# Performance work log

Hardware: AMD Instinct MI355X
Metric: run time of the kernel (lower is better)

## Reference

```python
import math
import jax, jax.numpy as jnp
import numpy as np
from jax import lax

B, T, D = 2, 2048, 1024
H, W, E = 16, 16, 8
HD = D // H


def setup_inputs() -> dict:
    key = jax.random.key(0)
    ks = jax.random.split(key, 9)
    s = 0.02
    return {
        "x": jax.random.normal(ks[0], (B, T, D), dtype=jnp.float32),
        # CausalConv1d weights: torch Conv1d layout [out_ch, in_ch, kernel]
        "q_w": jax.random.normal(ks[1], (D, D, W), dtype=jnp.float32) * s,
        "q_b": jax.random.normal(ks[2], (D,), dtype=jnp.float32) * s,
        "k_w": jax.random.normal(ks[3], (D, D, W), dtype=jnp.float32) * s,
        "k_b": jax.random.normal(ks[4], (D,), dtype=jnp.float32) * s,
        # Linear weights: torch layout [out, in]
        "v_w": jax.random.normal(ks[5], (D, D), dtype=jnp.float32) * s,
        "v_b": jax.random.normal(ks[6], (D,), dtype=jnp.float32) * s,
        "p_w": jax.random.normal(ks[7], (D, D), dtype=jnp.float32) * s,
        "p_b": jax.random.normal(ks[8], (D,), dtype=jnp.float32) * s,
    }


def _causal_conv(x_t, w, b):
    # x_t: [B, D, T]; left-pad by W-1 so output at t sees inputs <= t
    xp = jnp.pad(x_t, ((0, 0), (0, 0), (W - 1, 0)))
    y = lax.conv_general_dilated(xp, w, window_strides=(1,), padding="VALID",
                                 dimension_numbers=("NCH", "OIH", "NCH"))
    return y + b[None, :, None]


def _split_heads(z):
    # [B, T, D] -> [B, H, T, hd]
    return z.reshape(B, T, H, HD).transpose(0, 2, 1, 3)


def reference(x, q_w, q_b, k_w, k_b, v_w, v_b, p_w, p_b):
    x_t = x.transpose(0, 2, 1)  # [B, D, T]
    q = _split_heads(_causal_conv(x_t, q_w, q_b).transpose(0, 2, 1))
    k = _split_heads(_causal_conv(x_t, k_w, k_b).transpose(0, 2, 1))
    v = _split_heads(jnp.einsum("btd,od->bto", x, v_w) + v_b)
    scale = 1.0 / math.sqrt(HD)

    # ---- local window attention (unfold equivalent) ----
    # zero-pad keys/values W-1 steps to the left along T, gather sliding windows
    k_pad = jnp.pad(k, ((0, 0), (0, 0), (W - 1, 0), (0, 0)))
    v_pad = jnp.pad(v, ((0, 0), (0, 0), (W - 1, 0), (0, 0)))
    widx = jnp.arange(T)[:, None] + jnp.arange(W)[None, :]  # [T, W]
    patches_k = k_pad[:, :, widx]  # [B, H, T, W, hd]
    patches_v = v_pad[:, :, widx]  # [B, H, T, W, hd]
    attn_l = jax.nn.softmax(jnp.einsum("bhtd,bhtwd->bhtw", q, patches_k) * scale, axis=-1)
    out_l = jnp.einsum("bhtw,bhtwd->bhtd", attn_l, patches_v)

    # ---- exponential jumps: roll by 2^e (wrap-around, as in original) ----
    out_e = jnp.zeros_like(out_l)
    for e in range(E):
        shift = 2 ** e
        if shift >= T:
            break
        k_s = jnp.roll(k, -shift, axis=2)
        v_s = jnp.roll(v, -shift, axis=2)
        score = jnp.sum(q * k_s, axis=-1) * scale  # [B, H, T]
        alpha = jax.nn.softmax(score, axis=-1)[..., None]  # softmax over T (faithful)
        out_e = out_e + alpha * v_s

    out = (out_l + out_e).transpose(0, 2, 1, 3).reshape(B, T, D)
    return jnp.einsum("btd,od->bto", out, p_w) + p_b
```

## Files before the change

### kernel.cpp

```cpp
#include <hip/hip_runtime.h>
#include <cstdint>
#include <cstddef>

#define TSEQ 2048
#define DDIM 1024

typedef _Float16 f16;
typedef _Float16 f16x2 __attribute__((ext_vector_type(2)));
typedef _Float16 f16x4 __attribute__((ext_vector_type(4)));
typedef _Float16 f16x8 __attribute__((ext_vector_type(8)));
typedef float f32x4 __attribute__((ext_vector_type(4)));


__device__ __align__(16) static const unsigned char g_zero16[16] = {};

__device__ __forceinline__ void gload_lds16(const void* g, void* l) {
  __builtin_amdgcn_global_load_lds(
      (const __attribute__((address_space(1))) void*)g,
      (__attribute__((address_space(3))) void*)l, 16, 0, 0);
}

__global__ void cvt_all(const float* __restrict__ x, const float* __restrict__ vw,
                        const float* __restrict__ pw,
                        f16* __restrict__ xh, f16* __restrict__ vwh, f16* __restrict__ pwh) {
  int b = blockIdx.x;
  const float* src; f16* dst; int i;
  if (b < 4096)      { src = x;  dst = xh;  i = b * 256 + threadIdx.x; }
  else if (b < 5120) { src = vw; dst = vwh; i = (b - 4096) * 256 + threadIdx.x; }
  else               { src = pw; dst = pwh; i = (b - 5120) * 256 + threadIdx.x; }
  float4 v = ((const float4*)src)[i];
  f16x4 h = { (f16)v.x, (f16)v.y, (f16)v.z, (f16)v.w };
  ((f16x4*)dst)[i] = h;
}

__global__ __launch_bounds__(256) void cvt_w_tr(const float* __restrict__ qw,
                                                const float* __restrict__ kw,
                                                f16* __restrict__ qd, f16* __restrict__ kd) {
  __shared__ f16 tile[16][1032];
  const int o = blockIdx.x;
  const float* src; f16* dst;
  if (o < 1024) { src = qw + (size_t)o * 16384; dst = qd + (size_t)o * 16384; }
  else          { src = kw + (size_t)(o - 1024) * 16384; dst = kd + (size_t)(o - 1024) * 16384; }
  const int tid = threadIdx.x;
  #pragma unroll
  for (int p = 0; p < 16; p++) {
    const int idx = p * 256 + tid;
    const int i = idx >> 2, wq = idx & 3;
    float4 v = *(const float4*)(src + (size_t)i * 16 + wq * 4);
    tile[wq * 4 + 0][i] = (f16)v.x;
    tile[wq * 4 + 1][i] = (f16)v.y;
    tile[wq * 4 + 2][i] = (f16)v.z;
    tile[wq * 4 + 3][i] = (f16)v.w;
  }
  __syncthreads();
  #pragma unroll
  for (int p = 0; p < 8; p++) {
    const int c = p * 256 + tid;
    const int w = c >> 7, i8 = (c & 127) * 8;
    *(f16x8*)(dst + (size_t)w * 1024 + i8) = *(const f16x8*)&tile[w][i8];
  }
}

__global__ __launch_bounds__(512, 1) void gemm_qk8(
    const f16* __restrict__ xh,
    const f16* __restrict__ Bq, const f16* __restrict__ Bk,
    const float* __restrict__ bq, const float* __restrict__ bk,
    f16* __restrict__ oq, f16* __restrict__ ok)
{
  extern __shared__ __align__(16) f16 smem[];
  const int tid = threadIdx.x;
  const int lane = tid & 63;
  const int wid = tid >> 6;
  const int wq = wid >> 1;
  const int wp = wid & 1;

  const int m0 = blockIdx.x * 256;
  const int n0 = blockIdx.y * 64;
  const int bT = m0 & ~(TSEQ - 1);
  const int t0 = m0 & (TSEQ - 1);

  const int srow = lane >> 3;
  const int chunk8 = (((lane & 7) ^ (srow & 7)) << 3);

  f32x4 acc[4][4] = {};

  auto stageA = [&](int kt, int buf) {
    const int kk = kt << 6;
    const int w = kk >> 10;
    const int i0 = kk & (DDIM - 1);
    f16* sb = smem + buf * 24576;
    #pragma unroll
    for (int c = 0; c < 4; c++) {
      const int rr = wid * 32 + c * 8;
      const int srcT = t0 + rr + srow + w - 15;
      const void* g = (srcT >= 0)
          ? (const void*)(xh + (((size_t)(bT + srcT)) << 10) + i0 + chunk8)
          : (const void*)g_zero16;
      gload_lds16(g, (void*)&sb[rr * 64]);
    }
  };
  auto stageB = [&](int kt, int buf) {
    const int kk = kt << 6;
    f16* sb = smem + buf * 24576 + (wid < 4 ? 16384 : 20480);
    const f16* Bsrc = (wid < 4) ? Bq : Bk;
    const int wb = wid & 3;
    #pragma unroll
    for (int c = 0; c < 2; c++) {
      const int rr = wb * 16 + c * 8;
      const void* g = (const void*)(Bsrc + (((size_t)(n0 + rr + srow)) << 14) + kk + chunk8);
      gload_lds16(g, (void*)&sb[rr * 64]);
    }
  };

  stageA(0, 0); stageB(0, 0);
  stageA(1, 1); stageB(1, 1);

  const int NT = 16384 / 64;
  int buf = 0;
  for (int kt = 0; kt < NT; kt++) {
    if (kt < NT - 1) {
      asm volatile("s_waitcnt vmcnt(6)" ::: "memory");
    } else {
      asm volatile("s_waitcnt vmcnt(0)" ::: "memory");
    }
    __builtin_amdgcn_s_barrier();
    __builtin_amdgcn_sched_barrier(0);

    const f16* sb = smem + buf * 24576;
    const f16* bsb = sb + (wp ? 20480 : 16384);
    const int stq = kt + 2;
    const int sbuf = (buf >= 1) ? buf - 1 : 2;

    {
      const int slot = (((lane >> 4)) ^ (lane & 7)) << 3;
      f16x8 af[4], bf[4];
      #pragma unroll
      for (int i = 0; i < 4; i++)
        af[i] = *(const f16x8*)&sb[(wq * 64 + i * 16 + (lane & 15)) * 64 + slot];
      #pragma unroll
      for (int j = 0; j < 4; j++)
        bf[j] = *(const f16x8*)&bsb[(j * 16 + (lane & 15)) * 64 + slot];
      if (stq < NT) stageA(stq, sbuf);
      __builtin_amdgcn_s_barrier();
      asm volatile("s_waitcnt lgkmcnt(0)" ::: "memory");
      __builtin_amdgcn_sched_barrier(0);
      __builtin_amdgcn_s_setprio(1);
      #pragma unroll
      for (int i = 0; i < 4; i++)
        #pragma unroll
        for (int j = 0; j < 4; j++)
          acc[i][j] = __builtin_amdgcn_mfma_f32_16x16x32_f16(af[i], bf[j], acc[i][j], 0, 0, 0);
      __builtin_amdgcn_s_setprio(0);
    }

    {
      const int slot = ((4 + (lane >> 4)) ^ (lane & 7)) << 3;
      f16x8 af[4], bf[4];
      #pragma unroll
      for (int i = 0; i < 4; i++)
        af[i] = *(const f16x8*)&sb[(wq * 64 + i * 16 + (lane & 15)) * 64 + slot];
      #pragma unroll
      for (int j = 0; j < 4; j++)
        bf[j] = *(const f16x8*)&bsb[(j * 16 + (lane & 15)) * 64 + slot];
      if (stq < NT) stageB(stq, sbuf);
      __builtin_amdgcn_s_barrier();
      asm volatile("s_waitcnt lgkmcnt(0)" ::: "memory");
      __builtin_amdgcn_sched_barrier(0);
      __builtin_amdgcn_s_setprio(1);
      #pragma unroll
      for (int i = 0; i < 4; i++)
        #pragma unroll
        for (int j = 0; j < 4; j++)
          acc[i][j] = __builtin_amdgcn_mfma_f32_16x16x32_f16(af[i], bf[j], acc[i][j], 0, 0, 0);
      __builtin_amdgcn_s_setprio(0);
    }

    buf = (buf == 2) ? 0 : buf + 1;
  }

  const int crow = (lane >> 4) << 2;
  const int ccol = lane & 15;
  const int hh = n0 >> 6;
  const float* bias = wp ? bk : bq;
  f16* outp = wp ? ok : oq;
  #pragma unroll
  for (int j = 0; j < 4; j++) {
    const int col = n0 + j * 16 + ccol;
    const float bvl = bias[col];
    const int d = (j << 4) + ccol;
    #pragma unroll
    for (int i = 0; i < 4; i++) {
      #pragma unroll
      for (int r = 0; r < 4; r++) {
        const int row = m0 + wq * 64 + i * 16 + crow + r;
        const int b = row >> 11, t = row & (TSEQ - 1);
        outp[((size_t)(b * 16 + hh) * TSEQ + t) * 64 + d] = (f16)(acc[i][j][r] + bvl);
      }
    }
  }
}

template<int MODE>
__global__ __launch_bounds__(256, 2) void gemm_small(
    const f16* __restrict__ A, const f16* __restrict__ Bw,
    const float* __restrict__ bias, f16* __restrict__ oh, float* __restrict__ ofp)
{
  __shared__ f16 As[128 * 32];
  __shared__ f16 Bs[128 * 32];
  const int tid = threadIdx.x;
  const int lane = tid & 63;
  const int wid = tid >> 6;
  const int m0 = blockIdx.x * 128;
  const int n0 = blockIdx.y * 128;

  const int srow = lane >> 2;
  const int scg = ((lane & 3) ^ ((lane >> 3) & 3)) * 8;
  const int wm = wid & 1;
  const int wn = wid >> 1;

  f32x4 acc[4][4] = {};

  for (int kk = 0; kk < 1024; kk += 32) {
    __syncthreads();
    if (wid < 2) {
      #pragma unroll
      for (int c = 0; c < 4; c++) {
        const int r = wid * 64 + c * 16 + srow;
        const void* g = (const void*)(A + (((size_t)(m0 + r)) << 10) + kk + scg);
        gload_lds16(g, (void*)&As[(wid * 64 + c * 16) * 32]);
      }
    } else {
      #pragma unroll
      for (int c = 0; c < 4; c++) {
        const int r = (wid - 2) * 64 + c * 16 + srow;
        const void* g = (const void*)(Bw + (((size_t)(n0 + r)) << 10) + kk + scg);
        gload_lds16(g, (void*)&Bs[((wid - 2) * 64 + c * 16) * 32]);
      }
    }
    __syncthreads();
    const int koff = ((lane >> 4) ^ ((lane >> 1) & 3)) * 8;
    f16x8 af[4], bf[4];
    #pragma unroll
    for (int i = 0; i < 4; i++) {
      af[i] = *(const f16x8*)&As[(wm * 64 + i * 16 + (lane & 15)) * 32 + koff];
      bf[i] = *(const f16x8*)&Bs[(wn * 64 + i * 16 + (lane & 15)) * 32 + koff];
    }
    #pragma unroll
    for (int i = 0; i < 4; i++)
      #pragma unroll
      for (int j = 0; j < 4; j++)
        acc[i][j] = __builtin_amdgcn_mfma_f32_16x16x32_f16(af[i], bf[j], acc[i][j], 0, 0, 0);
  }

  const int crow = (lane >> 4) * 4;
  const int ccol = lane & 15;
  #pragma unroll
  for (int j = 0; j < 4; j++) {
    const int col = n0 + wn * 64 + j * 16 + ccol;
    const float bvl = bias[col];
    #pragma unroll
    for (int i = 0; i < 4; i++) {
      #pragma unroll
      for (int r = 0; r < 4; r++) {
        const int row = m0 + wm * 64 + i * 16 + crow + r;
        const float val = acc[i][j][r] + bvl;
        if (MODE == 1) {
          ofp[(size_t)row * DDIM + col] = val;
        } else {
          const int b = row >> 11, t = row & (TSEQ - 1);
          const int h = col >> 6, d = col & 63;
          oh[((size_t)(b * 16 + h) * TSEQ + t) * 64 + d] = (f16)val;
        }
      }
    }
  }
}

__global__ __launch_bounds__(256) void score_k(const f16* __restrict__ qh,
                                               const f16* __restrict__ kh,
                                               float* __restrict__ scores) {
  const int bid = blockIdx.x;
  const int bh = bid >> 5, tc = bid & 31;
  const int tid = threadIdx.x;
  const int wave = tid >> 6, lane = tid & 63;
  const int tr = lane >> 3, dc = lane & 7;
  const size_t base = ((size_t)bh) << 17;
  const f16* qb = qh + base;
  const f16* kb = kh + base;

  #pragma unroll
  for (int p = 0; p < 2; p++) {
    const int t = tc * 64 + p * 32 + wave * 8 + tr;
    f16x8 qv = *(const f16x8*)(qb + (size_t)t * 64 + dc * 8);
    const f16x2* qp = (const f16x2*)&qv;
    #pragma unroll
    for (int e = 0; e < 8; e++) {
      const int ts = (t + (1 << e)) & (TSEQ - 1);
      f16x8 kv = *(const f16x8*)(kb + (size_t)ts * 64 + dc * 8);
      const f16x2* kp = (const f16x2*)&kv;
      float s = 0.f;
      #pragma unroll
      for (int j = 0; j < 4; j++) s = __builtin_amdgcn_fdot2(qp[j], kp[j], s, false);
      s += __shfl_xor(s, 1, 64);
      s += __shfl_xor(s, 2, 64);
      s += __shfl_xor(s, 4, 64);
      if (dc == 0) scores[((size_t)(bh * 8 + e) << 11) + t] = s * 0.125f;
    }
  }
}

__global__ void softmax_k(float* __restrict__ scores) {
  __shared__ float red[4];
  int row = blockIdx.x;
  float* p = scores + ((size_t)row << 11);
  int tid = threadIdx.x;
  float v[8];
  float4 a = ((const float4*)p)[tid * 2];
  float4 b = ((const float4*)p)[tid * 2 + 1];
  v[0] = a.x; v[1] = a.y; v[2] = a.z; v[3] = a.w;
  v[4] = b.x; v[5] = b.y; v[6] = b.z; v[7] = b.w;
  float m = v[0];
  #pragma unroll
  for (int j = 1; j < 8; j++) m = fmaxf(m, v[j]);
  for (int o = 32; o > 0; o >>= 1) m = fmaxf(m, __shfl_xor(m, o, 64));
  if ((tid & 63) == 0) red[tid >> 6] = m;
  __syncthreads();
  m = fmaxf(fmaxf(red[0], red[1]), fmaxf(red[2], red[3]));
  __syncthreads();
  float s = 0.f;
  #pragma unroll
  for (int j = 0; j < 8; j++) { v[j] = __expf(v[j] - m); s += v[j]; }
  for (int o = 32; o > 0; o >>= 1) s += __shfl_xor(s, o, 64);
  if ((tid & 63) == 0) red[tid >> 6] = s;
  __syncthreads();
  s = (red[0] + red[1]) + (red[2] + red[3]);
  float inv = 1.0f / s;
  float4 o1 = make_float4(v[0] * inv, v[1] * inv, v[2] * inv, v[3] * inv);
  float4 o2 = make_float4(v[4] * inv, v[5] * inv, v[6] * inv, v[7] * inv);
  ((float4*)p)[tid * 2] = o1;
  ((float4*)p)[tid * 2 + 1] = o2;
}

__global__ __launch_bounds__(256) void attn_out_k(
    const f16* __restrict__ qh, const f16* __restrict__ kh, const f16* __restrict__ vh,
    const float* __restrict__ alpha, f16* __restrict__ outh)
{
  __shared__ f16 qL[64 * 64];
  __shared__ f16 kL[80 * 64];
  __shared__ f16 vL[208 * 64];
  __shared__ float scL[64 * 16];
  __shared__ float aL[8 * 64];
  const int bh = blockIdx.x, tc = blockIdx.y;
  const int t0 = tc * 64;
  const int tid = threadIdx.x;
  const size_t base = ((size_t)bh) << 17;

  for (int idx = tid; idx < 64 * 8; idx += 256) {
    int r = idx >> 3, c = idx & 7, sl = c ^ (r & 7);
    *(uint4*)&qL[r * 64 + sl * 8] = *(const uint4*)(qh + base + (size_t)(t0 + r) * 64 + c * 8);
  }
  for (int idx = tid; idx < 79 * 8; idx += 256) {
    int r = idx >> 3, c = idx & 7, sl = c ^ (r & 7);
    int g = t0 - 15 + r;
    uint4 val = (g < 0) ? make_uint4(0, 0, 0, 0)
                        : *(const uint4*)(kh + base + (size_t)g * 64 + c * 8);
    *(uint4*)&kL[r * 64 + sl * 8] = val;
  }
  for (int idx = tid; idx < 207 * 8; idx += 256) {
    int r = idx >> 3, c = idx & 7, sl = c ^ (r & 7);
    int g = t0 - 15 + r;
    uint4 val;
    if (g < 0) val = make_uint4(0, 0, 0, 0);
    else {
      if (g >= TSEQ) g -= TSEQ;
      val = *(const uint4*)(vh + base + (size_t)g * 64 + c * 8);
    }
    *(uint4*)&vL[r * 64 + sl * 8] = val;
  }
  for (int idx = tid; idx < 512; idx += 256) {
    int e = idx >> 6, i = idx & 63;
    aL[e * 64 + i] = alpha[((size_t)(bh * 8 + e) << 11) + t0 + i];
  }
  __syncthreads();

  {
    const int tl = tid & 63;
    const int wg = tid >> 6;
    f16x8 qv[8];
    #pragma unroll
    for (int c = 0; c < 8; c++) qv[c] = *(const f16x8*)&qL[tl * 64 + ((c ^ (tl & 7)) * 8)];
    const f16x2* qp = (const f16x2*)&qv[0];
    #pragma unroll
    for (int wi = 0; wi < 4; wi++) {
      const int w = wg * 4 + wi;
      const int r = tl + w;
      float s = 0.f;
      #pragma unroll
      for (int c = 0; c < 8; c++) {
        f16x8 kv = *(const f16x8*)&kL[r * 64 + ((c ^ (r & 7)) * 8)];
        const f16x2* kp = (const f16x2*)&kv;
        #pragma unroll
        for (int j = 0; j < 4; j++) s = __builtin_amdgcn_fdot2(qp[c * 4 + j], kp[j], s, false);
      }
      scL[tl * 16 + w] = s * 0.125f;
    }
  }
  __syncthreads();

  if (tid < 64) {
    float sc[16];
    float m = -1e30f;
    #pragma unroll
    for (int w = 0; w < 16; w++) { sc[w] = scL[tid * 16 + w]; m = fmaxf(m, sc[w]); }
    float sum = 0.f;
    #pragma unroll
    for (int w = 0; w < 16; w++) { sc[w] = __expf(sc[w] - m); sum += sc[w]; }
    float inv = 1.0f / sum;
    #pragma unroll
    for (int w = 0; w < 16; w++) scL[tid * 16 + w] = sc[w] * inv;
  }
  __syncthreads();

  {
    const int tl = tid >> 2;
    const int qd = tid & 3;
    float accv[16] = {};
    #pragma unroll
    for (int w = 0; w < 16; w++) {
      const float pw_ = scL[tl * 16 + w];
      const int r = tl + w;
      #pragma unroll
      for (int c2 = 0; c2 < 2; c2++) {
        const int c = qd * 2 + c2;
        f16x8 v = *(const f16x8*)&vL[r * 64 + ((c ^ (r & 7)) * 8)];
        #pragma unroll
        for (int j = 0; j < 8; j++) accv[c2 * 8 + j] += pw_ * (float)v[j];
      }
    }
    #pragma unroll
    for (int e = 0; e < 8; e++) {
      const float a = aL[e * 64 + tl];
      const int r = tl + 15 + (1 << e);
      #pragma unroll
      for (int c2 = 0; c2 < 2; c2++) {
        const int c = qd * 2 + c2;
        f16x8 v = *(const f16x8*)&vL[r * 64 + ((c ^ (r & 7)) * 8)];
        #pragma unroll
        for (int j = 0; j < 8; j++) accv[c2 * 8 + j] += a * (float)v[j];
      }
    }
    const int b = bh >> 4, h = bh & 15;
    f16* orow = outh + ((size_t)(b * TSEQ + t0 + tl)) * DDIM + h * 64 + qd * 16;
    #pragma unroll
    for (int c2 = 0; c2 < 2; c2++) {
      f16x8 v;
      #pragma unroll
      for (int j = 0; j < 8; j++) v[j] = (f16)accv[c2 * 8 + j];
      *(f16x8*)(orow + c2 * 8) = v;
    }
  }
}

extern "C" void kernel_launch(void* const* d_in, const int* in_sizes, int n_in,
                              void* d_out, int out_size, void* d_ws, size_t ws_size,
                              hipStream_t stream) {
  (void)in_sizes; (void)n_in; (void)out_size; (void)ws_size;
  const float* x   = (const float*)d_in[0];
  const float* q_w = (const float*)d_in[1];
  const float* q_b = (const float*)d_in[2];
  const float* k_w = (const float*)d_in[3];
  const float* k_b = (const float*)d_in[4];
  const float* v_w = (const float*)d_in[5];
  const float* v_b = (const float*)d_in[6];
  const float* p_w = (const float*)d_in[7];
  const float* p_b = (const float*)d_in[8];
  float* out = (float*)d_out;

  char* ws = (char*)d_ws;
  f16* xh      = (f16*)(ws);
  f16* qwh     = (f16*)(ws + 8388608);
  f16* kwh     = (f16*)(ws + 41943040);
  f16* vwh     = (f16*)(ws + 75497472);
  f16* pwh     = (f16*)(ws + 77594624);
  f16* qh      = (f16*)(ws + 79691776);
  f16* kh      = (f16*)(ws + 88080384);
  f16* vh      = (f16*)(ws + 96468992);
  f16* outh    = (f16*)(ws + 104857600);
  float* alpha = (float*)(ws + 113246208);

  static int s_attr_done = 0;
  if (!s_attr_done) {
    hipFuncSetAttribute((const void*)gemm_qk8,
                        hipFuncAttributeMaxDynamicSharedMemorySize, 147456);
    s_attr_done = 1;
  }

  cvt_all<<<6144, 256, 0, stream>>>(x, v_w, p_w, xh, vwh, pwh);
  cvt_w_tr<<<2048, 256, 0, stream>>>(q_w, k_w, qwh, kwh);

  gemm_qk8<<<dim3(16, 16), 512, 147456, stream>>>(xh, qwh, kwh, q_b, k_b, qh, kh);
  gemm_small<0><<<dim3(32, 8), 256, 0, stream>>>(xh, vwh, v_b, vh, nullptr);

  score_k<<<1024, 256, 0, stream>>>(qh, kh, alpha);
  softmax_k<<<256, 256, 0, stream>>>(alpha);
  attn_out_k<<<dim3(32, 32), 256, 0, stream>>>(qh, kh, vh, alpha, outh);

  gemm_small<1><<<dim3(32, 8), 256, 0, stream>>>(outh, pwh, p_b, nullptr, out);
}
```

Baseline: 517.3 us.

## Reorder conv-GEMM to reuse shifted X tile across taps and prefragment weights

The QK causal-conv GEMM now loops over 64-wide input-channel blocks and loads one X tile of 272 rows into LDS. All 16 conv taps reuse it by shifting the row index, instead of restaging X for every (tap, channel) K-slice. Weights are pre-permuted by a new conversion kernel into MFMA fragment order so each lane reads its B operands directly from global into registers, double-buffered, skipping LDS for B. Blocks are also remapped so each XCD handles the same N-blocks, which improves L2 locality. The risks are higher register pressure and B loads coming straight from global memory with only one k-step of prefetch lead.

```diff
diff --git a/kernel.cpp b/kernel.cpp
--- a/kernel.cpp
+++ b/kernel.cpp
@@ -33,37 +33,52 @@
   ((f16x4*)dst)[i] = h;
 }
 
-__global__ __launch_bounds__(256) void cvt_w_tr(const float* __restrict__ qw,
-                                                const float* __restrict__ kw,
-                                                f16* __restrict__ qd, f16* __restrict__ kd) {
-  __shared__ f16 tile[16][1032];
-  const int o = blockIdx.x;
+__global__ __launch_bounds__(256) void cvt_w_frag(const float* __restrict__ qw,
+                                                  const float* __restrict__ kw,
+                                                  f16* __restrict__ qd, f16* __restrict__ kd) {
+  extern __shared__ f16 wt_lds[];
+  const int bid = blockIdx.x;
   const float* src; f16* dst;
-  if (o < 1024) { src = qw + (size_t)o * 16384; dst = qd + (size_t)o * 16384; }
-  else          { src = kw + (size_t)(o - 1024) * 16384; dst = kd + (size_t)(o - 1024) * 16384; }
+  int o0;
+  if (bid < 256) { src = qw; dst = qd; o0 = bid * 4; }
+  else           { src = kw; dst = kd; o0 = (bid - 256) * 4; }
   const int tid = threadIdx.x;
-  #pragma unroll
-  for (int p = 0; p < 16; p++) {
+  for (int p = 0; p < 64; p++) {
     const int idx = p * 256 + tid;
-    const int i = idx >> 2, wq = idx & 3;
-    float4 v = *(const float4*)(src + (size_t)i * 16 + wq * 4);
-    tile[wq * 4 + 0][i] = (f16)v.x;
-    tile[wq * 4 + 1][i] = (f16)v.y;
-    tile[wq * 4 + 2][i] = (f16)v.z;
-    tile[wq * 4 + 3][i] = (f16)v.w;
-  }
-  __syncthreads();
-  #pragma unroll
-  for (int p = 0; p < 8; p++) {
-    const int c = p * 256 + tid;
-    const int w = c >> 7, i8 = (c & 127) * 8;
-    *(f16x8*)(dst + (size_t)w * 1024 + i8) = *(const f16x8*)&tile[w][i8];
+    const int ro = idx >> 12;
+    const int rem = idx & 4095;
+    const int i = rem >> 2, wq2 = rem & 3;
+    float4 v = *(const float4*)(src + (size_t)(o0 + ro) * 16384 + (size_t)i * 16 + wq2 * 4);
+    f16* trow = wt_lds + ro * 16512 + i;
+    trow[(wq2 * 4 + 0) * 1032] = (f16)v.x;
+    trow[(wq2 * 4 + 1) * 1032] = (f16)v.y;
+    trow[(wq2 * 4 + 2) * 1032] = (f16)v.z;
+    trow[(wq2 * 4 + 3) * 1032] = (f16)v.w;
+  }
+  __syncthreads();
+  const int jj = (o0 >> 4) & 3;
+  const int nb = o0 >> 6;
+  for (int p8 = 0; p8 < 8; p8++) {
+    const int p = p8 * 256 + tid;
+    const int ktp = p >> 3;
+    const int s = (p >> 2) & 1;
+    const int lhi = p & 3;
+    const int w = ktp & 15;
+    const int ibb = ktp >> 4;
+    const int i0 = ibb * 64 + s * 32 + lhi * 8;
+    const size_t dbase = (((size_t)(nb * 256 + ktp)) * 8 + jj * 2 + s) * 512;
+    #pragma unroll
+    for (int ro = 0; ro < 4; ro++) {
+      const int l = lhi * 16 + ((o0 + ro) & 15);
+      *(f16x8*)(dst + dbase + l * 8) =
+          *(const f16x8*)&wt_lds[ro * 16512 + w * 1032 + i0];
+    }
   }
 }
 
 __global__ __launch_bounds__(512, 1) void gemm_qk8(
     const f16* __restrict__ xh,
-    const f16* __restrict__ Bq, const f16* __restrict__ Bk,
+    const f16* __restrict__ Wfq, const f16* __restrict__ Wfk,
     const float* __restrict__ bq, const float* __restrict__ bk,
     f16* __restrict__ oq, f16* __restrict__ ok)
 {
@@ -74,108 +89,91 @@
   const int wq = wid >> 1;
   const int wp = wid & 1;
 
-  const int m0 = blockIdx.x * 256;
-  const int n0 = blockIdx.y * 64;
+  const int flat = blockIdx.y * 16 + blockIdx.x;
+  const int xcd = flat & 7;
+  const int idx = flat >> 3;
+  const int nblk = xcd * 2 + (idx >> 4);
+  const int mblk = idx & 15;
+  const int m0 = mblk * 256;
+  const int n0 = nblk * 64;
   const int bT = m0 & ~(TSEQ - 1);
   const int t0 = m0 & (TSEQ - 1);
 
   const int srow = lane >> 3;
   const int chunk8 = (((lane & 7) ^ (srow & 7)) << 3);
 
+  const f16* Wf = wp ? Wfk : Wfq;
+  const f16* wbase = Wf + ((size_t)nblk << 20) + lane * 8;
+
   f32x4 acc[4][4] = {};
-
-  auto stageA = [&](int kt, int buf) {
-    const int kk = kt << 6;
-    const int w = kk >> 10;
-    const int i0 = kk & (DDIM - 1);
-    f16* sb = smem + buf * 24576;
-    #pragma unroll
-    for (int c = 0; c < 4; c++) {
-      const int rr = wid * 32 + c * 8;
-      const int srcT = t0 + rr + srow + w - 15;
-      const void* g = (srcT >= 0)
-          ? (const void*)(xh + (((size_t)(bT + srcT)) << 10) + i0 + chunk8)
-          : (const void*)g_zero16;
-      gload_lds16(g, (void*)&sb[rr * 64]);
+  f16x8 bfr[2][8];
+
+  auto stageX = [&](int ib2, int bufp) {
+    f16* sb = smem + bufp * 17408;
+    const int ic = ib2 * 64 + chunk8;
+    #pragma unroll
+    for (int c = 0; c < 5; c++) {
+      const int g = c * 8 + wid;
+      if (g < 34) {
+        const int srcT = t0 + g * 8 + srow - 15;
+        const void* gp = (srcT >= 0)
+            ? (const void*)(xh + (((size_t)(bT + srcT)) << 10) + ic)
+            : (const void*)g_zero16;
+        gload_lds16(gp, (void*)&sb[g * 512]);
+      }
     }
   };
-  auto stageB = [&](int kt, int buf) {
-    const int kk = kt << 6;
-    f16* sb = smem + buf * 24576 + (wid < 4 ? 16384 : 20480);
-    const f16* Bsrc = (wid < 4) ? Bq : Bk;
-    const int wb = wid & 3;
-    #pragma unroll
-    for (int c = 0; c < 2; c++) {
-      const int rr = wb * 16 + c * 8;
-      const void* g = (const void*)(Bsrc + (((size_t)(n0 + rr + srow)) << 14) + kk + chunk8);
-      gload_lds16(g, (void*)&sb[rr * 64]);
-    }
+
+  auto loadB = [&](int kt, f16x8* bf) {
+    const f16* p = wbase + ((size_t)kt << 12);
+    #pragma unroll
+    for (int f = 0; f < 8; f++)
+      bf[f] = *(const f16x8*)(p + f * 512);
   };
 
-  stageA(0, 0); stageB(0, 0);
-  stageA(1, 1); stageB(1, 1);
-
-  const int NT = 16384 / 64;
-  int buf = 0;
-  for (int kt = 0; kt < NT; kt++) {
-    if (kt < NT - 1) {
-      asm volatile("s_waitcnt vmcnt(6)" ::: "memory");
-    } else {
-      asm volatile("s_waitcnt vmcnt(0)" ::: "memory");
-    }
-    __builtin_amdgcn_s_barrier();
+  stageX(0, 0);
+  loadB(0, bfr[0]);
+  asm volatile("s_waitcnt vmcnt(0)" ::: "memory");
+  __builtin_amdgcn_s_barrier();
+  __builtin_amdgcn_sched_barrier(0);
+
+  for (int ib = 0; ib < 16; ib++) {
+    if (ib > 0) {
+      __builtin_amdgcn_s_barrier();
+      __builtin_amdgcn_sched_barrier(0);
+    }
+    if (ib + 1 < 16) stageX(ib + 1, (ib + 1) & 1);
     __builtin_amdgcn_sched_barrier(0);
-
-    const f16* sb = smem + buf * 24576;
-    const f16* bsb = sb + (wp ? 20480 : 16384);
-    const int stq = kt + 2;
-    const int sbuf = (buf >= 1) ? buf - 1 : 2;
-
-    {
-      const int slot = (((lane >> 4)) ^ (lane & 7)) << 3;
-      f16x8 af[4], bf[4];
-      #pragma unroll
-      for (int i = 0; i < 4; i++)
-        af[i] = *(const f16x8*)&sb[(wq * 64 + i * 16 + (lane & 15)) * 64 + slot];
-      #pragma unroll
-      for (int j = 0; j < 4; j++)
-        bf[j] = *(const f16x8*)&bsb[(j * 16 + (lane & 15)) * 64 + slot];
-      if (stq < NT) stageA(stq, sbuf);
-      __builtin_amdgcn_s_barrier();
-      asm volatile("s_waitcnt lgkmcnt(0)" ::: "memory");
-      __builtin_amdgcn_sched_barrier(0);
+    const f16* xb = smem + (ib & 1) * 17408;
+    #pragma unroll
+    for (int wt = 0; wt < 16; wt++) {
+      const int kt = ib * 16 + wt;
+      const int rx = ((lane & 7) + wt) & 7;
+      const int sl0 = (((lane >> 4)) ^ rx) << 3;
+      const int sl1 = (((lane >> 4) + 4) ^ rx) << 3;
+      f16x8 af[8];
+      #pragma unroll
+      for (int i = 0; i < 4; i++) {
+        const int row = wq * 64 + i * 16 + (lane & 15) + wt;
+        af[i]     = *(const f16x8*)&xb[row * 64 + sl0];
+        af[4 + i] = *(const f16x8*)&xb[row * 64 + sl1];
+      }
+      if (kt + 1 < 256) loadB(kt + 1, bfr[(wt & 1) ^ 1]);
       __builtin_amdgcn_s_setprio(1);
       #pragma unroll
       for (int i = 0; i < 4; i++)
         #pragma unroll
         for (int j = 0; j < 4; j++)
-          acc[i][j] = __builtin_amdgcn_mfma_f32_16x16x32_f16(af[i], bf[j], acc[i][j], 0, 0, 0);
-      __builtin_amdgcn_s_setprio(0);
-    }
-
-    {
-      const int slot = ((4 + (lane >> 4)) ^ (lane & 7)) << 3;
-      f16x8 af[4], bf[4];
-      #pragma unroll
-      for (int i = 0; i < 4; i++)
-        af[i] = *(const f16x8*)&sb[(wq * 64 + i * 16 + (lane & 15)) * 64 + slot];
-      #pragma unroll
-      for (int j = 0; j < 4; j++)
-        bf[j] = *(const f16x8*)&bsb[(j * 16 + (lane & 15)) * 64 + slot];
-      if (stq < NT) stageB(stq, sbuf);
-      __builtin_amdgcn_s_barrier();
-      asm volatile("s_waitcnt lgkmcnt(0)" ::: "memory");
-      __builtin_amdgcn_sched_barrier(0);
-      __builtin_amdgcn_s_setprio(1);
+          acc[i][j] = __builtin_amdgcn_mfma_f32_16x16x32_f16(
+              af[i], bfr[wt & 1][2 * j], acc[i][j], 0, 0, 0);
       #pragma unroll
       for (int i = 0; i < 4; i++)
         #pragma unroll
         for (int j = 0; j < 4; j++)
-          acc[i][j] = __builtin_amdgcn_mfma_f32_16x16x32_f16(af[i], bf[j], acc[i][j], 0, 0, 0);
+          acc[i][j] = __builtin_amdgcn_mfma_f32_16x16x32_f16(
+              af[4 + i], bfr[wt & 1][2 * j + 1], acc[i][j], 0, 0, 0);
       __builtin_amdgcn_s_setprio(0);
     }
-
-    buf = (buf == 2) ? 0 : buf + 1;
   }
 
   const int crow = (lane >> 4) << 2;
@@ -491,14 +489,16 @@
   static int s_attr_done = 0;
   if (!s_attr_done) {
     hipFuncSetAttribute((const void*)gemm_qk8,
-                        hipFuncAttributeMaxDynamicSharedMemorySize, 147456);
+                        hipFuncAttributeMaxDynamicSharedMemorySize, 69632);
+    hipFuncSetAttribute((const void*)cvt_w_frag,
+                        hipFuncAttributeMaxDynamicSharedMemorySize, 132096);
     s_attr_done = 1;
   }
 
   cvt_all<<<6144, 256, 0, stream>>>(x, v_w, p_w, xh, vwh, pwh);
-  cvt_w_tr<<<2048, 256, 0, stream>>>(q_w, k_w, qwh, kwh);
-
-  gemm_qk8<<<dim3(16, 16), 512, 147456, stream>>>(xh, qwh, kwh, q_b, k_b, qh, kh);
+  cvt_w_frag<<<512, 256, 132096, stream>>>(q_w, k_w, qwh, kwh);
+
+  gemm_qk8<<<dim3(16, 16), 512, 69632, stream>>>(xh, qwh, kwh, q_b, k_b, qh, kh);
   gemm_small<0><<<dim3(32, 8), 256, 0, stream>>>(xh, vwh, v_b, vh, nullptr);
 
   score_k<<<1024, 256, 0, stream>>>(qh, kh, alpha);
```

New measurement: 488.9 us. 1.06x faster.
